# Performance work log

Measured on AMD Instinct MI355X. Metric: run time of the kernel, lower is better.

The kernel has to match this reference:

```python
import jax, jax.numpy as jnp
import numpy as np

NUM_TOKENS = 2048
HIDDEN = 1024
INTER = 2048
NUM_EXPERTS = 8
TOPK = 2


def setup_inputs() -> dict:
    key = jax.random.key(0)
    k1, k2, k3, k4 = jax.random.split(key, 4)
    hidden_states = jax.random.normal(k1, (NUM_TOKENS, HIDDEN), dtype=jnp.float32)
    router_logits = jax.random.normal(k2, (NUM_TOKENS, NUM_EXPERTS), dtype=jnp.float32)
    # fc1: [E, hidden, 2*intermediate] (proj/gate for SwiGLU), fc2: [E, intermediate, hidden]
    w1 = jax.random.normal(k3, (NUM_EXPERTS, HIDDEN, 2 * INTER), dtype=jnp.float32) * 0.02
    w2 = jax.random.normal(k4, (NUM_EXPERTS, INTER, HIDDEN), dtype=jnp.float32) * 0.02
    return {"hidden_states": hidden_states, "router_logits": router_logits, "w1": w1, "w2": w2}


def _grouped_gemm(x, w, expert_ids):
    """x: [T, D], w: [E, D, O], expert_ids: [T] -> [T, O].
    Tokens are routed to expert expert_ids[t]; equivalent to the sequential
    per-expert GEMM on contiguously sorted tokens. Small fixed loop over E."""
    out = jnp.zeros((x.shape[0], w.shape[-1]), dtype=x.dtype)
    for e in range(w.shape[0]):
        mask = (expert_ids == e)[:, None]
        out = out + jnp.where(mask, x, 0.0) @ w[e]
    return out


def reference(hidden_states, router_logits, w1, w2):
    # top-k routing + softmax over the selected logits
    top_logits, top_idx = jax.lax.top_k(router_logits, TOPK)      # [N, K]
    scores = jax.nn.softmax(top_logits, axis=-1)                  # [N, K]

    flat_idx = top_idx.reshape(-1)                                # [N*K]
    sorted_indices = jnp.argsort(flat_idx)                        # permute tokens grouped by expert
    permuted = hidden_states[sorted_indices // TOPK]              # [N*K, D]
    sorted_experts = flat_idx[sorted_indices]                     # [N*K] expert id per permuted row

    fc1_out = _grouped_gemm(permuted, w1, sorted_experts)         # [N*K, 2*I]
    proj, gate = jnp.split(fc1_out, 2, axis=-1)
    act = jax.nn.silu(proj) * gate                                # SwiGLU
    expert_out = _grouped_gemm(act, w2, sorted_experts)           # [N*K, D]

    # unpermute (scatter back) and weighted combine over top-k
    unpermuted = jnp.zeros_like(expert_out).at[sorted_indices].set(expert_out)
    unpermuted = unpermuted.reshape(-1, TOPK, expert_out.shape[-1])
    return (unpermuted * scores[..., None]).sum(axis=1)           # [N, D]
```

## Files before the change

kernel.cpp:

```cpp
#include <hip/hip_runtime.h>
#include <hip/hip_bf16.h>

constexpr int T = 2048;
constexpr int H = 1024;
constexpr int I = 2048;
constexpr int N2 = 2 * I;
constexpr int RCAP = 5120;
constexpr int MAXT = 40;

constexpr int WS_OFF = 16;
constexpr int WS_TEXP = 32;
constexpr int WS_TOPKP = 4256;
constexpr int WS_ROWTOK = 8352;
constexpr int WS_TOKROW = 13472;
constexpr size_t WSB_ZROW = 114688;
constexpr size_t WSB_HSB  = 131072;
constexpr size_t WSB_ACT  = 8u << 20;
constexpr size_t WSB_PW1  = 32u << 20;
constexpr size_t WSB_PW2  = 96u << 20;

constexpr int W1T_BLKS = 8 * 32 * 8;
constexpr int W2T_BLKS = 8 * 64 * 2;
constexpr int HSB_BLKS = T * H / 2048;
constexpr int FC1_BLKS = 32 * MAXT;

typedef __attribute__((ext_vector_type(4))) float f32x4;
typedef __attribute__((ext_vector_type(8))) short s16x8;

__device__ __forceinline__ short f2bf(float f) {
    unsigned u = __float_as_uint(f);
    u += 0x7FFFu + ((u >> 16) & 1u);
    return (short)(u >> 16);
}

#define MFMA16(a, b, c) __builtin_amdgcn_mfma_f32_16x16x32_bf16(a, b, c, 0, 0, 0)

__device__ __forceinline__ void gl2lds16(const void* g, void* l) {
    __builtin_amdgcn_global_load_lds(
        (const __attribute__((address_space(1))) void*)g,
        (__attribute__((address_space(3))) void*)l, 16, 0, 0);
}

__global__ __launch_bounds__(256) void pre_kernel(const float* __restrict__ logits,
                                                  int* __restrict__ wsi,
                                                  float* __restrict__ wsf,
                                                  const float* __restrict__ hs,
                                                  unsigned short* __restrict__ hsb,
                                                  const float* __restrict__ w1,
                                                  unsigned short* __restrict__ pw1) {
    __shared__ __align__(16) unsigned short L[32 * 512];
    const int t = threadIdx.x;

    if (blockIdx.x < W1T_BLKS) {
        int b = blockIdx.x;
        int cs = b & 7, k0i = (b >> 3) & 31, e = b >> 8;
        const float* src = w1 + (size_t)e * H * N2 + (size_t)(k0i * 32) * N2 + cs * 512;
        #pragma unroll
        for (int i = 0; i < 8; i++) {
            int c = t + i * 256;
            int row = c >> 6, col8 = (c & 63) * 8;
            const float* sp = src + (size_t)row * N2 + col8;
            f32x4 a = *(const f32x4*)sp;
            f32x4 bb = *(const f32x4*)(sp + 4);
            s16x8 s = {f2bf(a[0]), f2bf(a[1]), f2bf(a[2]), f2bf(a[3]),
                       f2bf(bb[0]), f2bf(bb[1]), f2bf(bb[2]), f2bf(bb[3])};
            *(s16x8*)&L[c * 8] = s;
        }
        __syncthreads();
        int gate = cs >> 2;
        int ctbase = (cs & 3) * 8;
        unsigned short* dstb = pw1 + (size_t)(e * 1024 + k0i) * 4096;
        #pragma unroll
        for (int i = 0; i < 8; i++) {
            int cidx = t + i * 256;
            int within = cidx & 31, nhalf = (cidx >> 5) & 1;
            int kg = (cidx >> 6) & 3, ctp = cidx >> 8;
            int x = ctp * 64 + nhalf * 32 + within;
            int n = gate * 32 + nhalf * 64 + within;
            s16x8 s;
            #pragma unroll
            for (int kk = 0; kk < 8; kk++) s[kk] = (short)L[(kg * 8 + kk) * 512 + x];
            int ct = ctbase + ctp;
            *(s16x8*)(dstb + (size_t)ct * 32 * 4096 + (kg * 128 + n) * 8) = s;
        }
        return;
    }
    if (blockIdx.x > W1T_BLKS) {
        int i = (((int)blockIdx.x - W1T_BLKS - 1) * 256 + t) * 8;
        f32x4 a = *(const f32x4*)(hs + i);
        f32x4 b = *(const f32x4*)(hs + i + 4);
        s16x8 s = {f2bf(a[0]), f2bf(a[1]), f2bf(a[2]), f2bf(a[3]),
                   f2bf(b[0]), f2bf(b[1]), f2bf(b[2]), f2bf(b[3])};
        *(s16x8*)(hsb + i) = s;
        return;
    }

    int* cnt  = (int*)L;
    int* base = cnt + 8;
    int* fill = base + 9;
    if (t < 8) { cnt[t] = 0; fill[t] = 0; }
    for (int r = t; r < RCAP; r += 256) wsi[WS_ROWTOK + r] = -1;
    unsigned short* zr = (unsigned short*)((char*)wsi + WSB_ZROW);
    for (int i = t; i < H; i += 256) zr[i] = 0;
    __syncthreads();

    int e0a[8], e1a[8];
    #pragma unroll
    for (int j = 0; j < 8; j++) {
        int tok = t * 8 + j;
        const float* l = logits + tok * 8;
        float v0 = -1e30f; int i0 = 0;
        #pragma unroll
        for (int i = 0; i < 8; i++) { float v = l[i]; if (v > v0) { v0 = v; i0 = i; } }
        float v1 = -1e30f; int i1 = 0;
        #pragma unroll
        for (int i = 0; i < 8; i++) { if (i == i0) continue; float v = l[i]; if (v > v1) { v1 = v; i1 = i; } }
        float ex = __expf(v1 - v0);
        float inv = 1.f / (1.f + ex);
        wsf[WS_TOPKP + tok * 2] = inv;
        wsf[WS_TOPKP + tok * 2 + 1] = ex * inv;
        e0a[j] = i0; e1a[j] = i1;
        atomicAdd(&cnt[i0], 1);
        atomicAdd(&cnt[i1], 1);
    }
    __syncthreads();
    if (t == 0) {
        int acc = 0;
        for (int e = 0; e < 8; e++) { base[e] = acc; acc += (cnt[e] + 127) & ~127; }
        base[8] = acc;
        for (int e = 0; e < 9; e++) wsi[WS_OFF + e] = base[e];
    }
    __syncthreads();
    for (int tt = t; tt < MAXT; tt += 256) {
        int rb = tt * 128, ex = 0;
        for (int e = 0; e < 8; e++)
            if (rb >= base[e] && rb < base[e + 1]) ex = e;
        wsi[WS_TEXP + tt] = ex;
    }
    #pragma unroll
    for (int j = 0; j < 8; j++) {
        int tok = t * 8 + j;
        int ee[2] = {e0a[j], e1a[j]};
        #pragma unroll
        for (int k = 0; k < 2; k++) {
            int e = ee[k];
            int slot = atomicAdd(&fill[e], 1);
            int r = base[e] + slot;
            wsi[WS_ROWTOK + r] = tok;
            wsi[WS_TOKROW + tok * 2 + k] = r;
        }
    }
}

__global__ __launch_bounds__(256, 4) void fc1_kernel(
    const unsigned short* __restrict__ hsb, const unsigned short* __restrict__ pw1,
    const int* __restrict__ wsi, const unsigned short* __restrict__ zrow,
    unsigned short* __restrict__ act,
    const float* __restrict__ w2, unsigned short* __restrict__ pw2) {
    __shared__ __align__(16) unsigned short SM[32 * 512];
    const int t = threadIdx.x;

    if (blockIdx.x >= FC1_BLKS) {
        int b = (int)blockIdx.x - FC1_BLKS;
        int cs = b & 1, k0i = (b >> 1) & 63, e = b >> 7;
        const float* src = w2 + (size_t)e * I * H + (size_t)(k0i * 32) * H + cs * 512;
        #pragma unroll
        for (int i = 0; i < 8; i++) {
            int c = t + i * 256;
            int row = c >> 6, col8 = (c & 63) * 8;
            const float* sp = src + (size_t)row * H + col8;
            f32x4 a = *(const f32x4*)sp;
            f32x4 bb = *(const f32x4*)(sp + 4);
            s16x8 s = {f2bf(a[0]), f2bf(a[1]), f2bf(a[2]), f2bf(a[3]),
                       f2bf(bb[0]), f2bf(bb[1]), f2bf(bb[2]), f2bf(bb[3])};
            *(s16x8*)&SM[c * 8] = s;
        }
        __syncthreads();
        unsigned short* dstb = pw2 + (size_t)(e * 512 + k0i) * 4096;
        #pragma unroll
        for (int i = 0; i < 8; i++) {
            int cidx = t + i * 256;
            int n = cidx & 127, kg = (cidx >> 7) & 3, htp = cidx >> 9;
            int x = htp * 128 + n;
            s16x8 s;
            #pragma unroll
            for (int kk = 0; kk < 8; kk++) s[kk] = (short)SM[(kg * 8 + kk) * 512 + x];
            int ht = cs * 4 + htp;
            *(s16x8*)(dstb + (size_t)ht * 64 * 4096 + (kg * 128 + n) * 8) = s;
        }
        return;
    }

    unsigned short* A0 = SM;
    unsigned short* B0 = SM + 4096;
    unsigned short* A1 = SM + 8192;
    unsigned short* B1 = SM + 12288;
    const int ct = blockIdx.x & 31, rt = blockIdx.x >> 5;
    const int rowb = rt * 128;
    if (rowb >= wsi[WS_OFF + 8]) return;
    const int e = wsi[WS_TEXP + rt];
    const unsigned short* pb = pw1 + (size_t)((e * 32 + ct) * 32) * 4096;

    const int m = t & 127;
    const int tok = wsi[WS_ROWTOK + rowb + m];
    const unsigned short* rp = (tok >= 0) ? (hsb + (size_t)tok * H) : zrow;
    const int kga = t >> 7;

    const int lane = t & 63, w = t >> 6, wr = w >> 1, wc = w & 1;
    const int q = lane >> 4, l16 = lane & 15;

    f32x4 zero = {0.f, 0.f, 0.f, 0.f};
    f32x4 acc[4][4];
    #pragma unroll
    for (int mi = 0; mi < 4; mi++)
        #pragma unroll
        for (int ni = 0; ni < 4; ni++) acc[mi][ni] = zero;

    #define FC1_STAGE(k0i, Ab, Bb)                                             \
        do {                                                                   \
            const int k0_ = (k0i) * 32;                                        \
            gl2lds16(rp + k0_ + kga * 8, &(Ab)[t * 8]);                        \
            gl2lds16(rp + k0_ + (kga + 2) * 8, &(Ab)[(t + 256) * 8]);          \
            const unsigned short* ps_ = pb + (size_t)(k0i) * 4096;             \
            gl2lds16(ps_ + t * 8, &(Bb)[t * 8]);                               \
            gl2lds16(ps_ + (t + 256) * 8, &(Bb)[(t + 256) * 8]);               \
        } while (0)

    #define FC1_COMPUTE(Ab, Bb)                                                \
        do {                                                                   \
            s16x8 af[4], bf[4];                                                \
            _Pragma("unroll")                                                  \
            for (int mi = 0; mi < 4; mi++)                                     \
                af[mi] = *(const s16x8*)&(Ab)[(q * 128 + wr * 64 + mi * 16 + l16) * 8]; \
            _Pragma("unroll")                                                  \
            for (int ni = 0; ni < 4; ni++)                                     \
                bf[ni] = *(const s16x8*)&(Bb)[(q * 128 + wc * 64 + ni * 16 + l16) * 8]; \
            _Pragma("unroll")                                                  \
            for (int mi = 0; mi < 4; mi++)                                     \
                _Pragma("unroll")                                              \
                for (int ni = 0; ni < 4; ni++)                                 \
                    acc[mi][ni] = MFMA16(af[mi], bf[ni], acc[mi][ni]);         \
        } while (0)

    FC1_STAGE(0, A0, B0);
    __syncthreads();
    for (int k0i = 0; k0i < 32; k0i += 2) {
        FC1_STAGE(k0i + 1, A1, B1);
        FC1_COMPUTE(A0, B0);
        __syncthreads();
        if (k0i + 2 < 32) FC1_STAGE(k0i + 2, A0, B0);
        FC1_COMPUTE(A1, B1);
        __syncthreads();
    }

    #pragma unroll
    for (int mi = 0; mi < 4; mi++)
        #pragma unroll
        for (int r = 0; r < 4; r++) {
            int row = rowb + wr * 64 + mi * 16 + q * 4 + r;
            #pragma unroll
            for (int ni = 0; ni < 2; ni++) {
                int col = ct * 64 + wc * 32 + ni * 16 + l16;
                float p = acc[mi][ni][r], g = acc[mi][ni + 2][r];
                float val = p * g / (1.f + __expf(-p));
                act[(size_t)row * I + col] = (unsigned short)f2bf(val);
            }
        }
}

__global__ __launch_bounds__(256, 4) void fc2_kernel(
    const unsigned short* __restrict__ act, const unsigned short* __restrict__ pw2,
    const int* __restrict__ wsi, float* __restrict__ eo) {
    __shared__ __align__(16) unsigned short SM[32 * 512];
    unsigned short* A0 = SM;
    unsigned short* B0 = SM + 4096;
    unsigned short* A1 = SM + 8192;
    unsigned short* B1 = SM + 12288;
    const int t = threadIdx.x;
    const int ht = blockIdx.x, rt = blockIdx.y, ks = blockIdx.z;
    const int rowb = rt * 128;
    if (rowb >= wsi[WS_OFF + 8]) return;
    const int e = wsi[WS_TEXP + rt];
    const unsigned short* pb = pw2 + (size_t)((e * 8 + ht) * 64) * 4096;

    const int m = t & 127;
    const unsigned short* rp = act + (size_t)(rowb + m) * I;
    const int kga = t >> 7;

    const int lane = t & 63, w = t >> 6, wr = w >> 1, wc = w & 1;
    const int q = lane >> 4, l16 = lane & 15;

    f32x4 zero = {0.f, 0.f, 0.f, 0.f};
    f32x4 acc[4][4];
    #pragma unroll
    for (int mi = 0; mi < 4; mi++)
        #pragma unroll
        for (int ni = 0; ni < 4; ni++) acc[mi][ni] = zero;

    #define FC2_STAGE(k0i, Ab, Bb)                                             \
        do {                                                                   \
            const int k0_ = (k0i) * 32;                                        \
            gl2lds16(rp + k0_ + kga * 8, &(Ab)[t * 8]);                        \
            gl2lds16(rp + k0_ + (kga + 2) * 8, &(Ab)[(t + 256) * 8]);          \
            const unsigned short* ps_ = pb + (size_t)(k0i) * 4096;             \
            gl2lds16(ps_ + t * 8, &(Bb)[t * 8]);                               \
            gl2lds16(ps_ + (t + 256) * 8, &(Bb)[(t + 256) * 8]);               \
        } while (0)

    #define FC2_COMPUTE(Ab, Bb)                                                \
        do {                                                                   \
            s16x8 af[4], bf[4];                                                \
            _Pragma("unroll")                                                  \
            for (int mi = 0; mi < 4; mi++)                                     \
                af[mi] = *(const s16x8*)&(Ab)[(q * 128 + wr * 64 + mi * 16 + l16) * 8]; \
            _Pragma("unroll")                                                  \
            for (int ni = 0; ni < 4; ni++)                                     \
                bf[ni] = *(const s16x8*)&(Bb)[(q * 128 + wc * 64 + ni * 16 + l16) * 8]; \
            _Pragma("unroll")                                                  \
            for (int mi = 0; mi < 4; mi++)                                     \
                _Pragma("unroll")                                              \
                for (int ni = 0; ni < 4; ni++)                                 \
                    acc[mi][ni] = MFMA16(af[mi], bf[ni], acc[mi][ni]);         \
        } while (0)

    const int kb = ks * 32;
    FC2_STAGE(kb, A0, B0);
    __syncthreads();
    for (int j = 0; j < 32; j += 2) {
        FC2_STAGE(kb + j + 1, A1, B1);
        FC2_COMPUTE(A0, B0);
        __syncthreads();
        if (j + 2 < 32) FC2_STAGE(kb + j + 2, A0, B0);
        FC2_COMPUTE(A1, B1);
        __syncthreads();
    }

    float* ed = eo + (size_t)ks * RCAP * H;
    #pragma unroll
    for (int mi = 0; mi < 4; mi++)
        #pragma unroll
        for (int r = 0; r < 4; r++) {
            int row = rowb + wr * 64 + mi * 16 + q * 4 + r;
            #pragma unroll
            for (int ni = 0; ni < 4; ni++) {
                int col = ht * 128 + wc * 64 + ni * 16 + l16;
                ed[(size_t)row * H + col] = acc[mi][ni][r];
            }
        }
}

__global__ __launch_bounds__(256) void combine_kernel(
    const float* __restrict__ eo, const int* __restrict__ wsi,
    const float* __restrict__ wsf, float* __restrict__ out) {
    const int tok = blockIdx.x;
    const int r0 = wsi[WS_TOKROW + tok * 2], r1 = wsi[WS_TOKROW + tok * 2 + 1];
    const float s0 = wsf[WS_TOPKP + tok * 2], s1 = wsf[WS_TOPKP + tok * 2 + 1];
    const float* a0 = eo + (size_t)r0 * H;
    const float* a1 = eo + (size_t)RCAP * H + (size_t)r0 * H;
    const float* b0 = eo + (size_t)r1 * H;
    const float* b1 = eo + (size_t)RCAP * H + (size_t)r1 * H;
    const int c = threadIdx.x * 4;
    f32x4 va0 = *(const f32x4*)(a0 + c), va1 = *(const f32x4*)(a1 + c);
    f32x4 vb0 = *(const f32x4*)(b0 + c), vb1 = *(const f32x4*)(b1 + c);
    f32x4 r;
    #pragma unroll
    for (int i = 0; i < 4; i++) r[i] = s0 * (va0[i] + va1[i]) + s1 * (vb0[i] + vb1[i]);
    *(f32x4*)(out + (size_t)tok * H + c) = r;
}

extern "C" void kernel_launch(void* const* d_in, const int* in_sizes, int n_in,
                              void* d_out, int out_size, void* d_ws, size_t ws_size,
                              hipStream_t stream) {
    const float* hs     = (const float*)d_in[0];
    const float* logits = (const float*)d_in[1];
    const float* w1     = (const float*)d_in[2];
    const float* w2     = (const float*)d_in[3];
    float* out = (float*)d_out;
    int* wsi = (int*)d_ws;
    float* wsf = (float*)d_ws;
    unsigned short* zrow = (unsigned short*)((char*)d_ws + WSB_ZROW);
    unsigned short* hsb  = (unsigned short*)((char*)d_ws + WSB_HSB);
    unsigned short* act  = (unsigned short*)((char*)d_ws + WSB_ACT);
    unsigned short* pw1  = (unsigned short*)((char*)d_ws + WSB_PW1);
    unsigned short* pw2  = (unsigned short*)((char*)d_ws + WSB_PW2);
    float* eo = (float*)((char*)d_ws + WSB_PW1);

    pre_kernel<<<W1T_BLKS + 1 + HSB_BLKS, 256, 0, stream>>>(logits, wsi, wsf, hs, hsb, w1, pw1);
    fc1_kernel<<<FC1_BLKS + W2T_BLKS, 256, 0, stream>>>(hsb, pw1, wsi, zrow, act, w2, pw2);
    fc2_kernel<<<dim3(8, MAXT, 2), 256, 0, stream>>>(act, pw2, wsi, eo);
    combine_kernel<<<T, 256, 0, stream>>>(eo, wsi, wsf, out);
}
```

Measured before the change: 367.3 us.

## Use direct global-to-LDS loads for weight conversion and vmcnt-based GEMM pipelining

The fc1 and fc2 main loops now issue two stages of global-to-LDS loads ahead and wait with partial s_waitcnt vmcnt(4) plus raw barriers instead of __syncthreads. This lets the next tile's loads stay in flight while the current tile is computed. The weight transpose/convert blocks now load fp32 directly into LDS via global_load_lds and convert to bf16 on readout, with twice as many blocks each covering half the columns. The vmcnt count assumes exactly four outstanding loads per stage, so correctness depends on the load counts hidden inside the stage macros.

```diff
diff --git a/kernel.cpp b/kernel.cpp
--- a/kernel.cpp
+++ b/kernel.cpp
@@ -19,8 +19,8 @@
 constexpr size_t WSB_PW1  = 32u << 20;
 constexpr size_t WSB_PW2  = 96u << 20;
 
-constexpr int W1T_BLKS = 8 * 32 * 8;
-constexpr int W2T_BLKS = 8 * 64 * 2;
+constexpr int W1T_BLKS = 8 * 32 * 16;
+constexpr int W2T_BLKS = 8 * 64 * 4;
 constexpr int HSB_BLKS = T * H / 2048;
 constexpr int FC1_BLKS = 32 * MAXT;
 
@@ -40,6 +40,15 @@
         (const __attribute__((address_space(1))) void*)g,
         (__attribute__((address_space(3))) void*)l, 16, 0, 0);
 }
+
+#define VM_WAIT4 asm volatile("s_waitcnt vmcnt(4)" ::: "memory")
+#define VM_WAIT0 asm volatile("s_waitcnt vmcnt(0)" ::: "memory")
+#define BARRIER                                     \
+    do {                                            \
+        asm volatile("" ::: "memory");              \
+        __builtin_amdgcn_s_barrier();               \
+        asm volatile("" ::: "memory");              \
+    } while (0)
 
 __global__ __launch_bounds__(256) void pre_kernel(const float* __restrict__ logits,
                                                   int* __restrict__ wsi,
@@ -48,40 +57,33 @@
                                                   unsigned short* __restrict__ hsb,
                                                   const float* __restrict__ w1,
                                                   unsigned short* __restrict__ pw1) {
-    __shared__ __align__(16) unsigned short L[32 * 512];
+    __shared__ __align__(16) float Lf[32 * 256];
     const int t = threadIdx.x;
 
     if (blockIdx.x < W1T_BLKS) {
         int b = blockIdx.x;
-        int cs = b & 7, k0i = (b >> 3) & 31, e = b >> 8;
-        const float* src = w1 + (size_t)e * H * N2 + (size_t)(k0i * 32) * N2 + cs * 512;
+        int cs = b & 15, k0i = (b >> 4) & 31, e = b >> 9;
+        const float* src = w1 + (size_t)e * H * N2 + (size_t)(k0i * 32) * N2 + cs * 256;
         #pragma unroll
         for (int i = 0; i < 8; i++) {
             int c = t + i * 256;
-            int row = c >> 6, col8 = (c & 63) * 8;
-            const float* sp = src + (size_t)row * N2 + col8;
-            f32x4 a = *(const f32x4*)sp;
-            f32x4 bb = *(const f32x4*)(sp + 4);
-            s16x8 s = {f2bf(a[0]), f2bf(a[1]), f2bf(a[2]), f2bf(a[3]),
-                       f2bf(bb[0]), f2bf(bb[1]), f2bf(bb[2]), f2bf(bb[3])};
-            *(s16x8*)&L[c * 8] = s;
+            int row = c >> 6, col4 = (c & 63) * 4;
+            gl2lds16(src + (size_t)row * N2 + col4, &Lf[c * 4]);
         }
         __syncthreads();
-        int gate = cs >> 2;
-        int ctbase = (cs & 3) * 8;
-        unsigned short* dstb = pw1 + (size_t)(e * 1024 + k0i) * 4096;
-        #pragma unroll
-        for (int i = 0; i < 8; i++) {
+        int gatebit = cs >> 3, csl = cs & 7;
+        #pragma unroll
+        for (int i = 0; i < 4; i++) {
             int cidx = t + i * 256;
-            int within = cidx & 31, nhalf = (cidx >> 5) & 1;
+            int within = cidx & 31, subh = (cidx >> 5) & 1;
             int kg = (cidx >> 6) & 3, ctp = cidx >> 8;
-            int x = ctp * 64 + nhalf * 32 + within;
-            int n = gate * 32 + nhalf * 64 + within;
+            int x = ctp * 64 + subh * 32 + within;
             s16x8 s;
             #pragma unroll
-            for (int kk = 0; kk < 8; kk++) s[kk] = (short)L[(kg * 8 + kk) * 512 + x];
-            int ct = ctbase + ctp;
-            *(s16x8*)(dstb + (size_t)ct * 32 * 4096 + (kg * 128 + n) * 8) = s;
+            for (int kk = 0; kk < 8; kk++) s[kk] = f2bf(Lf[(kg * 8 + kk) * 256 + x]);
+            int n = gatebit * 32 + subh * 64 + within;
+            int ct = csl * 4 + ctp;
+            *(s16x8*)(pw1 + ((size_t)(e * 32 + ct) * 32 + k0i) * 4096 + (kg * 128 + n) * 8) = s;
         }
         return;
     }
@@ -95,7 +97,7 @@
         return;
     }
 
-    int* cnt  = (int*)L;
+    int* cnt  = (int*)Lf;
     int* base = cnt + 8;
     int* fill = base + 9;
     if (t < 8) { cnt[t] = 0; fill[t] = 0; }
@@ -161,32 +163,27 @@
     const int t = threadIdx.x;
 
     if (blockIdx.x >= FC1_BLKS) {
+        float* Lf = (float*)SM;
         int b = (int)blockIdx.x - FC1_BLKS;
-        int cs = b & 1, k0i = (b >> 1) & 63, e = b >> 7;
-        const float* src = w2 + (size_t)e * I * H + (size_t)(k0i * 32) * H + cs * 512;
+        int cs = b & 3, k0i = (b >> 2) & 63, e = b >> 8;
+        const float* src = w2 + (size_t)e * I * H + (size_t)(k0i * 32) * H + cs * 256;
         #pragma unroll
         for (int i = 0; i < 8; i++) {
             int c = t + i * 256;
-            int row = c >> 6, col8 = (c & 63) * 8;
-            const float* sp = src + (size_t)row * H + col8;
-            f32x4 a = *(const f32x4*)sp;
-            f32x4 bb = *(const f32x4*)(sp + 4);
-            s16x8 s = {f2bf(a[0]), f2bf(a[1]), f2bf(a[2]), f2bf(a[3]),
-                       f2bf(bb[0]), f2bf(bb[1]), f2bf(bb[2]), f2bf(bb[3])};
-            *(s16x8*)&SM[c * 8] = s;
+            int row = c >> 6, col4 = (c & 63) * 4;
+            gl2lds16(src + (size_t)row * H + col4, &Lf[c * 4]);
         }
         __syncthreads();
-        unsigned short* dstb = pw2 + (size_t)(e * 512 + k0i) * 4096;
-        #pragma unroll
-        for (int i = 0; i < 8; i++) {
+        #pragma unroll
+        for (int i = 0; i < 4; i++) {
             int cidx = t + i * 256;
-            int n = cidx & 127, kg = (cidx >> 7) & 3, htp = cidx >> 9;
-            int x = htp * 128 + n;
+            int n = cidx & 127, kg = (cidx >> 7) & 3, h1 = cidx >> 9;
+            int x = h1 * 128 + n;
             s16x8 s;
             #pragma unroll
-            for (int kk = 0; kk < 8; kk++) s[kk] = (short)SM[(kg * 8 + kk) * 512 + x];
-            int ht = cs * 4 + htp;
-            *(s16x8*)(dstb + (size_t)ht * 64 * 4096 + (kg * 128 + n) * 8) = s;
+            for (int kk = 0; kk < 8; kk++) s[kk] = f2bf(Lf[(kg * 8 + kk) * 256 + x]);
+            int ht = cs * 2 + h1;
+            *(s16x8*)(pw2 + ((size_t)(e * 8 + ht) * 64 + k0i) * 4096 + (kg * 128 + n) * 8) = s;
         }
         return;
     }
@@ -243,15 +240,26 @@
         } while (0)
 
     FC1_STAGE(0, A0, B0);
-    __syncthreads();
-    for (int k0i = 0; k0i < 32; k0i += 2) {
-        FC1_STAGE(k0i + 1, A1, B1);
+    FC1_STAGE(1, A1, B1);
+    for (int k0i = 0; k0i < 30; k0i += 2) {
+        VM_WAIT4;
+        BARRIER;
         FC1_COMPUTE(A0, B0);
-        __syncthreads();
-        if (k0i + 2 < 32) FC1_STAGE(k0i + 2, A0, B0);
+        BARRIER;
+        FC1_STAGE(k0i + 2, A0, B0);
+        VM_WAIT4;
+        BARRIER;
         FC1_COMPUTE(A1, B1);
-        __syncthreads();
-    }
+        BARRIER;
+        FC1_STAGE(k0i + 3, A1, B1);
+    }
+    VM_WAIT4;
+    BARRIER;
+    FC1_COMPUTE(A0, B0);
+    BARRIER;
+    VM_WAIT0;
+    BARRIER;
+    FC1_COMPUTE(A1, B1);
 
     #pragma unroll
     for (int mi = 0; mi < 4; mi++)
@@ -325,15 +333,26 @@
 
     const int kb = ks * 32;
     FC2_STAGE(kb, A0, B0);
-    __syncthreads();
-    for (int j = 0; j < 32; j += 2) {
-        FC2_STAGE(kb + j + 1, A1, B1);
+    FC2_STAGE(kb + 1, A1, B1);
+    for (int j = 0; j < 30; j += 2) {
+        VM_WAIT4;
+        BARRIER;
         FC2_COMPUTE(A0, B0);
-        __syncthreads();
-        if (j + 2 < 32) FC2_STAGE(kb + j + 2, A0, B0);
+        BARRIER;
+        FC2_STAGE(kb + j + 2, A0, B0);
+        VM_WAIT4;
+        BARRIER;
         FC2_COMPUTE(A1, B1);
-        __syncthreads();
-    }
+        BARRIER;
+        FC2_STAGE(kb + j + 3, A1, B1);
+    }
+    VM_WAIT4;
+    BARRIER;
+    FC2_COMPUTE(A0, B0);
+    BARRIER;
+    VM_WAIT0;
+    BARRIER;
+    FC2_COMPUTE(A1, B1);
 
     float* ed = eo + (size_t)ks * RCAP * H;
     #pragma unroll
```

Result: faster. 353.8 us (-3.7%).
